# Kernel tuning notes

Measured on AMD Instinct MI355X. Metric: run time of the kernel, lower is better.

Reference implementation:

```python
import jax, jax.numpy as jnp
import numpy as np

B, D, H = 1024, 128, 512


def _made_masks(D, H):
    # Canonical MADE degrees with natural ordering.
    m_in = np.arange(1, D + 1)                       # input degrees 1..D
    m_hid = (np.arange(H) % (D - 1)) + 1             # hidden degrees in [1, D-1]
    m_out = np.concatenate([np.arange(1, D + 1)] * 2)  # output degrees, repeated for (sigma, mu)
    M1 = (m_hid[:, None] >= m_in[None, :]).astype(np.float32)   # [H, D]
    M2 = (m_out[:, None] > m_hid[None, :]).astype(np.float32)   # [2D, H]
    return jnp.asarray(M1), jnp.asarray(M2)


def setup_inputs() -> dict:
    key = jax.random.key(0)
    k1, k2, k3 = jax.random.split(key, 3)
    x = jax.random.normal(k1, (B, D), dtype=jnp.float32)
    # small init so exp(sigma) stays numerically tame
    W1 = jax.random.normal(k2, (H, D), dtype=jnp.float32) * 0.05
    b1 = jnp.zeros((H,), dtype=jnp.float32)
    W2 = jax.random.normal(k3, (2 * D, H), dtype=jnp.float32) * 0.05
    b2 = jnp.zeros((2 * D,), dtype=jnp.float32)
    return {"x": x, "W1": W1, "b1": b1, "W2": W2, "b2": b2}


def reference(x, W1, b1, W2, b2):
    Din = x.shape[1]
    Hid = W1.shape[0]
    M1, M2 = _made_masks(Din, Hid)

    def made(z):
        h = jax.nn.relu(z @ (W1 * M1).T + b1)   # [B, H]
        return h @ (W2 * M2).T + b2              # [B, 2D]

    # backward_flow: sequential inversion, one dim per step (kl_forward=True)
    def step(carry, d):
        z, log_det = carry
        res = made(z)
        sigma = res[:, :Din]
        mu = res[:, Din:]
        s_d = jnp.take(sigma, d, axis=1)
        m_d = jnp.take(mu, d, axis=1)
        x_d = jnp.take(x, d, axis=1)
        z = z.at[:, d].set((x_d - m_d) * jnp.exp(-s_d))
        return (z, log_det - s_d), None

    init = (jnp.zeros_like(x), jnp.zeros((x.shape[0],), dtype=x.dtype))
    (z, log_det), _ = jax.lax.scan(step, init, jnp.arange(Din))
    return z, log_det
```

## Files before the change

kernel.cpp:

```cpp
#include <hip/hip_runtime.h>


#define Bz  1024
#define Dd  128
#define Hh  512
#define HPL 8

typedef float v4f __attribute__((ext_vector_type(4)));

template<int CTRL, int RMASK>
__device__ __forceinline__ float dpp_add(float v) {
    int t = __builtin_amdgcn_update_dpp(0, __float_as_int(v), CTRL, RMASK, 0xf, true);
    return v + __int_as_float(t);
}
__device__ __forceinline__ float wave_sum_bcast(float v) {
    v = dpp_add<0x111, 0xf>(v);
    v = dpp_add<0x112, 0xf>(v);
    v = dpp_add<0x114, 0xf>(v);
    v = dpp_add<0x118, 0xf>(v);
    v = dpp_add<0x142, 0xa>(v);
    v = dpp_add<0x143, 0xc>(v);
    return __int_as_float(__builtin_amdgcn_readlane(__float_as_int(v), 63));
}
__device__ __forceinline__ float bcast_lane(float v, int l) {
    return __int_as_float(__builtin_amdgcn_readlane(__float_as_int(v), l));
}

__global__ void pack_kernel(const float* __restrict__ W1,
                            const float* __restrict__ W2,
                            float* __restrict__ Wp) {
    int idx = blockIdx.x * blockDim.x + threadIdx.x;
    if (idx >= Dd * Hh) return;
    int d = idx >> 9, h = idx & 511;
    int mh = (h % 127) + 1;
    float dot_on = (mh <= d) ? 1.f : 0.f;
    float upd_on = (mh >  d) ? 1.f : 0.f;
    float* bp = Wp + d * 1536;
    bp[h]        = W2[d * Hh + h] * dot_on;
    bp[512 + h]  = W2[(Dd + d) * Hh + h] * dot_on;
    bp[1024 + h] = W1[h * Dd + d] * upd_on;
}

struct WBuf { v4f s0, s1, m0, m1, w0, w1; };

__device__ __forceinline__ void loadbuf(WBuf &b, const float* p) {
    b.s0 = *(const v4f*)(p);
    b.s1 = *(const v4f*)(p + 4);
    b.m0 = *(const v4f*)(p + 512);
    b.m1 = *(const v4f*)(p + 516);
    b.w0 = *(const v4f*)(p + 1024);
    b.w1 = *(const v4f*)(p + 1028);
    __builtin_amdgcn_sched_barrier(0);
}

__device__ __forceinline__ void stepD(int d, int lane,
    float (&a)[HPL], const WBuf &w,
    float xa, float xb, float b2a, float b2b, float b2c, float b2d_,
    float &za, float &zb, float &ld)
{
    float ps0 = 0.f, ps1 = 0.f, pm0 = 0.f, pm1 = 0.f;
#pragma unroll
    for (int k = 0; k < 4; ++k) {
        float h = fmaxf(a[k], 0.f);
        ps0 = fmaf(h, w.s0[k], ps0);
        pm0 = fmaf(h, w.m0[k], pm0);
    }
#pragma unroll
    for (int k = 0; k < 4; ++k) {
        float h = fmaxf(a[4 + k], 0.f);
        ps1 = fmaf(h, w.s1[k], ps1);
        pm1 = fmaf(h, w.m1[k], pm1);
    }
    float ps = wave_sum_bcast(ps0 + ps1);
    float pm = wave_sum_bcast(pm0 + pm1);

    int dl = d & 63;
    float sd = ps + bcast_lane(d < 64 ? b2a : b2b, dl);
    float md = pm + bcast_lane(d < 64 ? b2c : b2d_, dl);
    float xv =      bcast_lane(d < 64 ? xa  : xb,  dl);
    float zd = (xv - md) * __expf(-sd);
    ld -= sd;
    if (dl == lane) { if (d < 64) za = zd; else zb = zd; }

#pragma unroll
    for (int k = 0; k < 4; ++k) a[k]     = fmaf(zd, w.w0[k], a[k]);
#pragma unroll
    for (int k = 0; k < 4; ++k) a[4 + k] = fmaf(zd, w.w1[k], a[4 + k]);
}

__global__ __launch_bounds__(64, 1) void iaf4_kernel(
    const float* __restrict__ x,
    const float* __restrict__ b1,
    const float* __restrict__ b2,
    const float* __restrict__ Wp,
    float* __restrict__ out)
{
    const int lane = (int)threadIdx.x;
    const int row  = (int)blockIdx.x;
    const int h0   = lane * HPL;

    float a[HPL];
    {
        float4 t0 = *(const float4*)(b1 + h0);
        float4 t1 = *(const float4*)(b1 + h0 + 4);
        a[0]=t0.x; a[1]=t0.y; a[2]=t0.z; a[3]=t0.w;
        a[4]=t1.x; a[5]=t1.y; a[6]=t1.z; a[7]=t1.w;
    }
    float xa  = x[row * Dd + lane];
    float xb  = x[row * Dd + 64 + lane];
    float b2a = b2[lane],       b2b = b2[64 + lane];
    float b2c = b2[128 + lane], b2d_ = b2[192 + lane];

    float za = 0.f, zb = 0.f, ld = 0.f;

    const float* base = Wp + h0;
    WBuf A, B, C, D;
    loadbuf(A, base + 0 * 1536);
    loadbuf(B, base + 1 * 1536);
    loadbuf(C, base + 2 * 1536);
    loadbuf(D, base + 3 * 1536);

#pragma unroll 1
    for (int t = 0; t < Dd; t += 4) {
        stepD(t + 0, lane, a, A, xa, xb, b2a, b2b, b2c, b2d_, za, zb, ld);
        loadbuf(A, base + (size_t)((t + 4 < Dd) ? (t + 4) : 0) * 1536);
        stepD(t + 1, lane, a, B, xa, xb, b2a, b2b, b2c, b2d_, za, zb, ld);
        loadbuf(B, base + (size_t)((t + 5 < Dd) ? (t + 5) : 1) * 1536);
        stepD(t + 2, lane, a, C, xa, xb, b2a, b2b, b2c, b2d_, za, zb, ld);
        loadbuf(C, base + (size_t)((t + 6 < Dd) ? (t + 6) : 2) * 1536);
        stepD(t + 3, lane, a, D, xa, xb, b2a, b2b, b2c, b2d_, za, zb, ld);
        loadbuf(D, base + (size_t)((t + 7 < Dd) ? (t + 7) : 3) * 1536);
    }

    out[row * Dd + lane]      = za;
    out[row * Dd + 64 + lane] = zb;
    if (lane == 0) out[Bz * Dd + row] = ld;
}

__global__ __launch_bounds__(64, 1) void iaf_fb_kernel(
    const float* __restrict__ x,  const float* __restrict__ W1,
    const float* __restrict__ b1, const float* __restrict__ W2,
    const float* __restrict__ b2, float* __restrict__ out)
{
    const int lane = (int)threadIdx.x;
    const int row  = (int)blockIdx.x;
    const int h0   = lane * HPL;
    float a[HPL]; int mh[HPL];
#pragma unroll
    for (int k = 0; k < HPL; ++k) { a[k] = b1[h0 + k]; mh[k] = ((h0 + k) % 127) + 1; }
    float xa  = x[row * Dd + lane], xb = x[row * Dd + 64 + lane];
    float b2a = b2[lane], b2b = b2[64 + lane], b2c = b2[128 + lane], b2d_ = b2[192 + lane];
    float za = 0.f, zb = 0.f, ld = 0.f;
    for (int d = 0; d < Dd; ++d) {
        float ps = 0.f, pm = 0.f;
#pragma unroll
        for (int k = 0; k < HPL; ++k) {
            float h = fmaxf(a[k], 0.f);
            h = (mh[k] <= d) ? h : 0.f;
            ps = fmaf(h, W2[d * Hh + h0 + k], ps);
            pm = fmaf(h, W2[(Dd + d) * Hh + h0 + k], pm);
        }
        ps = wave_sum_bcast(ps);
        pm = wave_sum_bcast(pm);
        int dl = d & 63;
        float sd = ps + bcast_lane(d < 64 ? b2a : b2b, dl);
        float md = pm + bcast_lane(d < 64 ? b2c : b2d_, dl);
        float xv =      bcast_lane(d < 64 ? xa  : xb,  dl);
        float zd = (xv - md) * __expf(-sd);
        ld -= sd;
        if (dl == lane) { if (d < 64) za = zd; else zb = zd; }
#pragma unroll
        for (int k = 0; k < HPL; ++k)
            if (d < mh[k]) a[k] = fmaf(zd, W1[(h0 + k) * Dd + d], a[k]);
    }
    out[row * Dd + lane]      = za;
    out[row * Dd + 64 + lane] = zb;
    if (lane == 0) out[Bz * Dd + row] = ld;
}

extern "C" void kernel_launch(void* const* d_in, const int* in_sizes, int n_in,
                              void* d_out, int out_size, void* d_ws, size_t ws_size,
                              hipStream_t stream) {
    const float* x  = (const float*)d_in[0];
    const float* W1 = (const float*)d_in[1];
    const float* b1 = (const float*)d_in[2];
    const float* W2 = (const float*)d_in[3];
    const float* b2 = (const float*)d_in[4];
    float* out = (float*)d_out;
    float* Wp  = (float*)d_ws;

    const size_t need = (size_t)Dd * 1536 * sizeof(float);
    if (ws_size >= need) {
        pack_kernel<<<(Dd * Hh + 255) / 256, 256, 0, stream>>>(W1, W2, Wp);
        iaf4_kernel<<<Bz, 64, 0, stream>>>(x, b1, b2, Wp, out);
    } else {
        iaf_fb_kernel<<<Bz, 64, 0, stream>>>(x, W1, b1, W2, b2, out);
    }
}
```

Measured before the change: 38.72 us.

## Process two batch rows per wave and fold log2 scaling into packed weights

Each 64-lane block now handles two batch rows, so every packed weight load is reused for two independent sequential chains. The two chains interleave their reductions and FMAs, which should hide the latency of the DPP reductions. The sigma weights and biases are pre-scaled by -1/ln2 so the exponential becomes a raw exp2 and the sign flip disappears; log_det is rescaled by ln2 at the end. The cost is half as many blocks (512 on a large GPU, lowering parallelism), more registers per lane, and the prefetch depth drops from four steps to two.

```diff
diff --git a/kernel.cpp b/kernel.cpp
--- a/kernel.cpp
+++ b/kernel.cpp
@@ -5,6 +5,8 @@
 #define Dd  128
 #define Hh  512
 #define HPL 8
+#define LN2 0.6931471805599453f
+#define NEG_RCP_LN2 -1.4426950408889634f
 
 typedef float v4f __attribute__((ext_vector_type(4)));
 
@@ -36,7 +38,7 @@
     float dot_on = (mh <= d) ? 1.f : 0.f;
     float upd_on = (mh >  d) ? 1.f : 0.f;
     float* bp = Wp + d * 1536;
-    bp[h]        = W2[d * Hh + h] * dot_on;
+    bp[h]        = W2[d * Hh + h] * dot_on * NEG_RCP_LN2;
     bp[512 + h]  = W2[(Dd + d) * Hh + h] * dot_on;
     bp[1024 + h] = W1[h * Dd + d] * upd_on;
 }
@@ -53,42 +55,65 @@
     __builtin_amdgcn_sched_barrier(0);
 }
 
-__device__ __forceinline__ void stepD(int d, int lane,
-    float (&a)[HPL], const WBuf &w,
-    float xa, float xb, float b2a, float b2b, float b2c, float b2d_,
-    float &za, float &zb, float &ld)
+__device__ __forceinline__ void stepR2(int d, int lane,
+    float (&a0)[HPL], float (&a1)[HPL], const WBuf &w,
+    float xa0, float xb0, float xa1, float xb1,
+    float b2a, float b2b, float b2c, float b2d_,
+    float &za0, float &zb0, float &za1, float &zb1,
+    float &ld0, float &ld1)
 {
-    float ps0 = 0.f, ps1 = 0.f, pm0 = 0.f, pm1 = 0.f;
-#pragma unroll
-    for (int k = 0; k < 4; ++k) {
-        float h = fmaxf(a[k], 0.f);
-        ps0 = fmaf(h, w.s0[k], ps0);
-        pm0 = fmaf(h, w.m0[k], pm0);
-    }
-#pragma unroll
-    for (int k = 0; k < 4; ++k) {
-        float h = fmaxf(a[4 + k], 0.f);
-        ps1 = fmaf(h, w.s1[k], ps1);
-        pm1 = fmaf(h, w.m1[k], pm1);
-    }
-    float ps = wave_sum_bcast(ps0 + ps1);
-    float pm = wave_sum_bcast(pm0 + pm1);
+    float p00 = 0.f, p01 = 0.f, q00 = 0.f, q01 = 0.f;
+    float p10 = 0.f, p11 = 0.f, q10 = 0.f, q11 = 0.f;
+#pragma unroll
+    for (int k = 0; k < 4; ++k) {
+        float h0 = fmaxf(a0[k], 0.f);
+        float h1 = fmaxf(a1[k], 0.f);
+        p00 = fmaf(h0, w.s0[k], p00);  q00 = fmaf(h0, w.m0[k], q00);
+        p10 = fmaf(h1, w.s0[k], p10);  q10 = fmaf(h1, w.m0[k], q10);
+    }
+#pragma unroll
+    for (int k = 0; k < 4; ++k) {
+        float h0 = fmaxf(a0[4 + k], 0.f);
+        float h1 = fmaxf(a1[4 + k], 0.f);
+        p01 = fmaf(h0, w.s1[k], p01);  q01 = fmaf(h0, w.m1[k], q01);
+        p11 = fmaf(h1, w.s1[k], p11);  q11 = fmaf(h1, w.m1[k], q11);
+    }
+    float sp0 = wave_sum_bcast(p00 + p01);
+    float sm0 = wave_sum_bcast(q00 + q01);
+    float sp1 = wave_sum_bcast(p10 + p11);
+    float sm1 = wave_sum_bcast(q10 + q11);
 
     int dl = d & 63;
-    float sd = ps + bcast_lane(d < 64 ? b2a : b2b, dl);
-    float md = pm + bcast_lane(d < 64 ? b2c : b2d_, dl);
-    float xv =      bcast_lane(d < 64 ? xa  : xb,  dl);
-    float zd = (xv - md) * __expf(-sd);
-    ld -= sd;
-    if (dl == lane) { if (d < 64) za = zd; else zb = zd; }
-
-#pragma unroll
-    for (int k = 0; k < 4; ++k) a[k]     = fmaf(zd, w.w0[k], a[k]);
-#pragma unroll
-    for (int k = 0; k < 4; ++k) a[4 + k] = fmaf(zd, w.w1[k], a[4 + k]);
-}
-
-__global__ __launch_bounds__(64, 1) void iaf4_kernel(
+    float bs  = bcast_lane(d < 64 ? b2a : b2b, dl);
+    float bm  = bcast_lane(d < 64 ? b2c : b2d_, dl);
+    float xv0 = bcast_lane(d < 64 ? xa0 : xb0, dl);
+    float xv1 = bcast_lane(d < 64 ? xa1 : xb1, dl);
+
+    float s0 = sp0 + bs, s1 = sp1 + bs;
+    float m0 = sm0 + bm, m1 = sm1 + bm;
+    float e0 = __builtin_amdgcn_exp2f(s0);
+    float e1 = __builtin_amdgcn_exp2f(s1);
+    float zd0 = (xv0 - m0) * e0;
+    float zd1 = (xv1 - m1) * e1;
+    ld0 += s0;
+    ld1 += s1;
+    if (dl == lane) {
+        if (d < 64) { za0 = zd0; za1 = zd1; }
+        else        { zb0 = zd0; zb1 = zd1; }
+    }
+#pragma unroll
+    for (int k = 0; k < 4; ++k) {
+        a0[k] = fmaf(zd0, w.w0[k], a0[k]);
+        a1[k] = fmaf(zd1, w.w0[k], a1[k]);
+    }
+#pragma unroll
+    for (int k = 0; k < 4; ++k) {
+        a0[4 + k] = fmaf(zd0, w.w1[k], a0[4 + k]);
+        a1[4 + k] = fmaf(zd1, w.w1[k], a1[4 + k]);
+    }
+}
+
+__global__ __launch_bounds__(64, 1) void iaf5_kernel(
     const float* __restrict__ x,
     const float* __restrict__ b1,
     const float* __restrict__ b2,
@@ -96,45 +121,51 @@
     float* __restrict__ out)
 {
     const int lane = (int)threadIdx.x;
-    const int row  = (int)blockIdx.x;
+    const int r0   = (int)blockIdx.x * 2;
+    const int r1   = r0 + 1;
     const int h0   = lane * HPL;
 
-    float a[HPL];
+    float a0[HPL], a1[HPL];
     {
         float4 t0 = *(const float4*)(b1 + h0);
         float4 t1 = *(const float4*)(b1 + h0 + 4);
-        a[0]=t0.x; a[1]=t0.y; a[2]=t0.z; a[3]=t0.w;
-        a[4]=t1.x; a[5]=t1.y; a[6]=t1.z; a[7]=t1.w;
-    }
-    float xa  = x[row * Dd + lane];
-    float xb  = x[row * Dd + 64 + lane];
-    float b2a = b2[lane],       b2b = b2[64 + lane];
-    float b2c = b2[128 + lane], b2d_ = b2[192 + lane];
-
-    float za = 0.f, zb = 0.f, ld = 0.f;
+        a0[0]=t0.x; a0[1]=t0.y; a0[2]=t0.z; a0[3]=t0.w;
+        a0[4]=t1.x; a0[5]=t1.y; a0[6]=t1.z; a0[7]=t1.w;
+#pragma unroll
+        for (int k = 0; k < HPL; ++k) a1[k] = a0[k];
+    }
+    float xa0 = x[r0 * Dd + lane],      xb0 = x[r0 * Dd + 64 + lane];
+    float xa1 = x[r1 * Dd + lane],      xb1 = x[r1 * Dd + 64 + lane];
+    float b2a = b2[lane] * NEG_RCP_LN2;
+    float b2b = b2[64 + lane] * NEG_RCP_LN2;
+    float b2c = b2[128 + lane],         b2d_ = b2[192 + lane];
+
+    float za0 = 0.f, zb0 = 0.f, za1 = 0.f, zb1 = 0.f;
+    float ld0 = 0.f, ld1 = 0.f;
 
     const float* base = Wp + h0;
-    WBuf A, B, C, D;
-    loadbuf(A, base + 0 * 1536);
-    loadbuf(B, base + 1 * 1536);
-    loadbuf(C, base + 2 * 1536);
-    loadbuf(D, base + 3 * 1536);
+    WBuf A, B;
+    loadbuf(A, base);
+    loadbuf(B, base + 1536);
 
 #pragma unroll 1
-    for (int t = 0; t < Dd; t += 4) {
-        stepD(t + 0, lane, a, A, xa, xb, b2a, b2b, b2c, b2d_, za, zb, ld);
-        loadbuf(A, base + (size_t)((t + 4 < Dd) ? (t + 4) : 0) * 1536);
-        stepD(t + 1, lane, a, B, xa, xb, b2a, b2b, b2c, b2d_, za, zb, ld);
-        loadbuf(B, base + (size_t)((t + 5 < Dd) ? (t + 5) : 1) * 1536);
-        stepD(t + 2, lane, a, C, xa, xb, b2a, b2b, b2c, b2d_, za, zb, ld);
-        loadbuf(C, base + (size_t)((t + 6 < Dd) ? (t + 6) : 2) * 1536);
-        stepD(t + 3, lane, a, D, xa, xb, b2a, b2b, b2c, b2d_, za, zb, ld);
-        loadbuf(D, base + (size_t)((t + 7 < Dd) ? (t + 7) : 3) * 1536);
-    }
-
-    out[row * Dd + lane]      = za;
-    out[row * Dd + 64 + lane] = zb;
-    if (lane == 0) out[Bz * Dd + row] = ld;
+    for (int t = 0; t < Dd; t += 2) {
+        stepR2(t, lane, a0, a1, A, xa0, xb0, xa1, xb1,
+               b2a, b2b, b2c, b2d_, za0, zb0, za1, zb1, ld0, ld1);
+        loadbuf(A, base + (size_t)((t + 2 < Dd) ? (t + 2) : 0) * 1536);
+        stepR2(t + 1, lane, a0, a1, B, xa0, xb0, xa1, xb1,
+               b2a, b2b, b2c, b2d_, za0, zb0, za1, zb1, ld0, ld1);
+        loadbuf(B, base + (size_t)((t + 3 < Dd) ? (t + 3) : 1) * 1536);
+    }
+
+    out[r0 * Dd + lane]      = za0;
+    out[r0 * Dd + 64 + lane] = zb0;
+    out[r1 * Dd + lane]      = za1;
+    out[r1 * Dd + 64 + lane] = zb1;
+    if (lane == 0) {
+        out[Bz * Dd + r0] = LN2 * ld0;
+        out[Bz * Dd + r1] = LN2 * ld1;
+    }
 }
 
 __global__ __launch_bounds__(64, 1) void iaf_fb_kernel(
@@ -192,7 +223,7 @@
     const size_t need = (size_t)Dd * 1536 * sizeof(float);
     if (ws_size >= need) {
         pack_kernel<<<(Dd * Hh + 255) / 256, 256, 0, stream>>>(W1, W2, Wp);
-        iaf4_kernel<<<Bz, 64, 0, stream>>>(x, b1, b2, Wp, out);
+        iaf5_kernel<<<Bz / 2, 64, 0, stream>>>(x, b1, b2, Wp, out);
     } else {
         iaf_fb_kernel<<<Bz, 64, 0, stream>>>(x, W1, b1, W2, b2, out);
     }
```

Result: slower. 60.43 us (+56.1%).

## Stream packed weights through LDS via async global_load_lds with swizzled layout

Applied to the files above, without the earlier changes.

Replaces the register-buffered weight prefetch with a 4-deep LDS ring filled by direct global-to-LDS loads, waiting on vmcnt each step. The pack kernel now emits a swizzled layout so LDS reads avoid bank conflicts, and folds -log2(e) into the sigma weights and biases so exp becomes a native exp2 with the log-det rescaled once at the end. The aim is to free VGPRs and hide global-load latency in the serial 128-step loop. In exchange it depends on a hand-tuned waitcnt count and uses 24KB of LDS per block.

```diff
diff --git a/kernel.cpp b/kernel.cpp
--- a/kernel.cpp
+++ b/kernel.cpp
@@ -1,12 +1,16 @@
 #include <hip/hip_runtime.h>
+#include <stdint.h>
 
 
 #define Bz  1024
 #define Dd  128
 #define Hh  512
-#define HPL 8
+#define LN2 0.6931471805599453f
+#define NRL -1.4426950408889634f
 
 typedef float v4f __attribute__((ext_vector_type(4)));
+typedef const __attribute__((address_space(1))) uint32_t* gas_t;
+typedef __attribute__((address_space(3))) uint32_t* las_t;
 
 template<int CTRL, int RMASK>
 __device__ __forceinline__ float dpp_add(float v) {
@@ -30,76 +34,32 @@
                             const float* __restrict__ W2,
                             float* __restrict__ Wp) {
     int idx = blockIdx.x * blockDim.x + threadIdx.x;
-    if (idx >= Dd * Hh) return;
-    int d = idx >> 9, h = idx & 511;
+    if (idx >= Dd * 1536) return;
+    int d = idx / 1536, f = idx % 1536;
+    int seg = f >> 9, h = f & 511;
     int mh = (h % 127) + 1;
-    float dot_on = (mh <= d) ? 1.f : 0.f;
-    float upd_on = (mh >  d) ? 1.f : 0.f;
-    float* bp = Wp + d * 1536;
-    bp[h]        = W2[d * Hh + h] * dot_on;
-    bp[512 + h]  = W2[(Dd + d) * Hh + h] * dot_on;
-    bp[1024 + h] = W1[h * Dd + d] * upd_on;
-}
-
-struct WBuf { v4f s0, s1, m0, m1, w0, w1; };
-
-__device__ __forceinline__ void loadbuf(WBuf &b, const float* p) {
-    b.s0 = *(const v4f*)(p);
-    b.s1 = *(const v4f*)(p + 4);
-    b.m0 = *(const v4f*)(p + 512);
-    b.m1 = *(const v4f*)(p + 516);
-    b.w0 = *(const v4f*)(p + 1024);
-    b.w1 = *(const v4f*)(p + 1028);
-    __builtin_amdgcn_sched_barrier(0);
-}
-
-__device__ __forceinline__ void stepD(int d, int lane,
-    float (&a)[HPL], const WBuf &w,
-    float xa, float xb, float b2a, float b2b, float b2c, float b2d_,
-    float &za, float &zb, float &ld)
-{
-    float ps0 = 0.f, ps1 = 0.f, pm0 = 0.f, pm1 = 0.f;
-#pragma unroll
-    for (int k = 0; k < 4; ++k) {
-        float h = fmaxf(a[k], 0.f);
-        ps0 = fmaf(h, w.s0[k], ps0);
-        pm0 = fmaf(h, w.m0[k], pm0);
-    }
-#pragma unroll
-    for (int k = 0; k < 4; ++k) {
-        float h = fmaxf(a[4 + k], 0.f);
-        ps1 = fmaf(h, w.s1[k], ps1);
-        pm1 = fmaf(h, w.m1[k], pm1);
-    }
-    float ps = wave_sum_bcast(ps0 + ps1);
-    float pm = wave_sum_bcast(pm0 + pm1);
-
-    int dl = d & 63;
-    float sd = ps + bcast_lane(d < 64 ? b2a : b2b, dl);
-    float md = pm + bcast_lane(d < 64 ? b2c : b2d_, dl);
-    float xv =      bcast_lane(d < 64 ? xa  : xb,  dl);
-    float zd = (xv - md) * __expf(-sd);
-    ld -= sd;
-    if (dl == lane) { if (d < 64) za = zd; else zb = zd; }
-
-#pragma unroll
-    for (int k = 0; k < 4; ++k) a[k]     = fmaf(zd, w.w0[k], a[k]);
-#pragma unroll
-    for (int k = 0; k < 4; ++k) a[4 + k] = fmaf(zd, w.w1[k], a[4 + k]);
-}
-
-__global__ __launch_bounds__(64, 1) void iaf4_kernel(
+    float v;
+    if (seg == 0)      v = W2[d * Hh + h]        * ((mh <= d) ? NRL : 0.f);
+    else if (seg == 1) v = W2[(Dd + d) * Hh + h] * ((mh <= d) ? 1.f : 0.f);
+    else               v = W1[h * Dd + d]        * ((mh >  d) ? 1.f : 0.f);
+    int c = (f >> 2) & 127, e = f & 3;
+    int pos = (seg << 7) + (c & ~1) + ((c & 1) ^ ((c >> 3) & 1));
+    Wp[d * 1536 + pos * 4 + e] = v;
+}
+
+__global__ __launch_bounds__(64, 1) void iaf6_kernel(
     const float* __restrict__ x,
     const float* __restrict__ b1,
     const float* __restrict__ b2,
     const float* __restrict__ Wp,
     float* __restrict__ out)
 {
+    __shared__ float lds[4 * 1536];
     const int lane = (int)threadIdx.x;
     const int row  = (int)blockIdx.x;
-    const int h0   = lane * HPL;
-
-    float a[HPL];
+    const int h0   = lane * 8;
+
+    float a[8];
     {
         float4 t0 = *(const float4*)(b1 + h0);
         float4 t1 = *(const float4*)(b1 + h0 + 4);
@@ -108,33 +68,77 @@
     }
     float xa  = x[row * Dd + lane];
     float xb  = x[row * Dd + 64 + lane];
-    float b2a = b2[lane],       b2b = b2[64 + lane];
-    float b2c = b2[128 + lane], b2d_ = b2[192 + lane];
-
-    float za = 0.f, zb = 0.f, ld = 0.f;
-
-    const float* base = Wp + h0;
-    WBuf A, B, C, D;
-    loadbuf(A, base + 0 * 1536);
-    loadbuf(B, base + 1 * 1536);
-    loadbuf(C, base + 2 * 1536);
-    loadbuf(D, base + 3 * 1536);
+    float b2a = b2[lane] * NRL,        b2b = b2[64 + lane] * NRL;
+    float b2c = b2[128 + lane],        b2d_ = b2[192 + lane];
+    asm volatile("" : "+v"(xa), "+v"(xb), "+v"(b2a), "+v"(b2b), "+v"(b2c),
+                      "+v"(b2d_), "+v"(a[0]), "+v"(a[1]), "+v"(a[2]),
+                      "+v"(a[3]), "+v"(a[4]), "+v"(a[5]), "+v"(a[6]), "+v"(a[7]));
+
+    auto stage = [&](int t) {
+        const float* g = Wp + (size_t)t * 1536 + lane * 4;
+        float* lb = lds + (t & 3) * 1536;
+#pragma unroll
+        for (int i = 0; i < 6; ++i)
+            __builtin_amdgcn_global_load_lds((gas_t)(g + i * 256),
+                                             (las_t)(lb + i * 256), 16, 0, 0);
+    };
+
+    stage(0); stage(1); stage(2); stage(3);
+
+    float za = 0.f, zb = 0.f, ldet = 0.f;
+    const int bit = (lane >> 2) & 1;
+    const int p0  = 2 * lane + bit;
+    const int p1  = 2 * lane + 1 - bit;
 
 #pragma unroll 1
-    for (int t = 0; t < Dd; t += 4) {
-        stepD(t + 0, lane, a, A, xa, xb, b2a, b2b, b2c, b2d_, za, zb, ld);
-        loadbuf(A, base + (size_t)((t + 4 < Dd) ? (t + 4) : 0) * 1536);
-        stepD(t + 1, lane, a, B, xa, xb, b2a, b2b, b2c, b2d_, za, zb, ld);
-        loadbuf(B, base + (size_t)((t + 5 < Dd) ? (t + 5) : 1) * 1536);
-        stepD(t + 2, lane, a, C, xa, xb, b2a, b2b, b2c, b2d_, za, zb, ld);
-        loadbuf(C, base + (size_t)((t + 6 < Dd) ? (t + 6) : 2) * 1536);
-        stepD(t + 3, lane, a, D, xa, xb, b2a, b2b, b2c, b2d_, za, zb, ld);
-        loadbuf(D, base + (size_t)((t + 7 < Dd) ? (t + 7) : 3) * 1536);
+    for (int t = 0; t < Dd; ++t) {
+        asm volatile("s_waitcnt vmcnt(18)" ::: "memory");
+        __builtin_amdgcn_sched_barrier(0);
+
+        const v4f* lp = (const v4f*)(lds + (t & 3) * 1536);
+        v4f s0 = lp[p0],       s1 = lp[p1];
+        v4f m0 = lp[128 + p0], m1 = lp[128 + p1];
+        v4f w0 = lp[256 + p0], w1 = lp[256 + p1];
+
+        float ps0 = 0.f, ps1 = 0.f, pm0 = 0.f, pm1 = 0.f;
+#pragma unroll
+        for (int k = 0; k < 4; ++k) {
+            float hv = fmaxf(a[k], 0.f);
+            ps0 = fmaf(hv, s0[k], ps0);
+            pm0 = fmaf(hv, m0[k], pm0);
+        }
+#pragma unroll
+        for (int k = 0; k < 4; ++k) {
+            float hv = fmaxf(a[4 + k], 0.f);
+            ps1 = fmaf(hv, s1[k], ps1);
+            pm1 = fmaf(hv, m1[k], pm1);
+        }
+        float sp = wave_sum_bcast(ps0 + ps1);
+        float sm = wave_sum_bcast(pm0 + pm1);
+
+        int dl = t & 63;
+        float bs = bcast_lane(t < 64 ? b2a : b2b, dl);
+        float bm = bcast_lane(t < 64 ? b2c : b2d_, dl);
+        float xv = bcast_lane(t < 64 ? xa  : xb,  dl);
+
+        float sd = sp + bs;
+        float zd = (xv - (sm + bm)) * __builtin_amdgcn_exp2f(sd);
+        ldet += sd;
+        if (dl == lane) { if (t < 64) za = zd; else zb = zd; }
+
+#pragma unroll
+        for (int k = 0; k < 4; ++k) a[k]     = fmaf(zd, w0[k], a[k]);
+#pragma unroll
+        for (int k = 0; k < 4; ++k) a[4 + k] = fmaf(zd, w1[k], a[4 + k]);
+
+        __builtin_amdgcn_sched_barrier(0);
+        asm volatile("s_waitcnt lgkmcnt(0)" ::: "memory");
+        if (t < Dd - 4) stage(t + 4);
     }
 
     out[row * Dd + lane]      = za;
     out[row * Dd + 64 + lane] = zb;
-    if (lane == 0) out[Bz * Dd + row] = ld;
+    if (lane == 0) out[Bz * Dd + row] = LN2 * ldet;
 }
 
 __global__ __launch_bounds__(64, 1) void iaf_fb_kernel(
@@ -144,17 +148,17 @@
 {
     const int lane = (int)threadIdx.x;
     const int row  = (int)blockIdx.x;
-    const int h0   = lane * HPL;
-    float a[HPL]; int mh[HPL];
-#pragma unroll
-    for (int k = 0; k < HPL; ++k) { a[k] = b1[h0 + k]; mh[k] = ((h0 + k) % 127) + 1; }
+    const int h0   = lane * 8;
+    float a[8]; int mh[8];
+#pragma unroll
+    for (int k = 0; k < 8; ++k) { a[k] = b1[h0 + k]; mh[k] = ((h0 + k) % 127) + 1; }
     float xa  = x[row * Dd + lane], xb = x[row * Dd + 64 + lane];
     float b2a = b2[lane], b2b = b2[64 + lane], b2c = b2[128 + lane], b2d_ = b2[192 + lane];
     float za = 0.f, zb = 0.f, ld = 0.f;
     for (int d = 0; d < Dd; ++d) {
         float ps = 0.f, pm = 0.f;
 #pragma unroll
-        for (int k = 0; k < HPL; ++k) {
+        for (int k = 0; k < 8; ++k) {
             float h = fmaxf(a[k], 0.f);
             h = (mh[k] <= d) ? h : 0.f;
             ps = fmaf(h, W2[d * Hh + h0 + k], ps);
@@ -170,7 +174,7 @@
         ld -= sd;
         if (dl == lane) { if (d < 64) za = zd; else zb = zd; }
 #pragma unroll
-        for (int k = 0; k < HPL; ++k)
+        for (int k = 0; k < 8; ++k)
             if (d < mh[k]) a[k] = fmaf(zd, W1[(h0 + k) * Dd + d], a[k]);
     }
     out[row * Dd + lane]      = za;
@@ -191,8 +195,8 @@
 
     const size_t need = (size_t)Dd * 1536 * sizeof(float);
     if (ws_size >= need) {
-        pack_kernel<<<(Dd * Hh + 255) / 256, 256, 0, stream>>>(W1, W2, Wp);
-        iaf4_kernel<<<Bz, 64, 0, stream>>>(x, b1, b2, Wp, out);
+        pack_kernel<<<(Dd * 1536 + 255) / 256, 256, 0, stream>>>(W1, W2, Wp);
+        iaf6_kernel<<<Bz, 64, 0, stream>>>(x, b1, b2, Wp, out);
     } else {
         iaf_fb_kernel<<<Bz, 64, 0, stream>>>(x, W1, b1, W2, b2, out);
     }
```

Result: slower. 53.15 us (+37.3%).

## Fold biases and exp scaling into packed weights and use packed FMAs

Applied to the files above, without the earlier changes.

The pack kernel now pre-scales the sigma weights by -log2(e) and the W1 update weights by exp(-b2[d]). This lets the serial loop work in the base-2 domain with no per-step bias broadcasts, and the per-dim exp(-b2) factor and the log-det bias sum are applied once at the end. The inner dot and update loops are also rewritten with 2-wide vector FMAs so the compiler can emit packed fp32 instructions. Together these shorten the latency-bound serial chain per dimension, at the cost of slightly different floating-point rounding.

```diff
diff --git a/kernel.cpp b/kernel.cpp
--- a/kernel.cpp
+++ b/kernel.cpp
@@ -1,12 +1,18 @@
 #include <hip/hip_runtime.h>
+#include <stdint.h>
 
 
 #define Bz  1024
 #define Dd  128
 #define Hh  512
-#define HPL 8
+#define LN2 0.6931471805599453f
+#define NRL -1.4426950408889634f
 
 typedef float v4f __attribute__((ext_vector_type(4)));
+typedef float v2f __attribute__((ext_vector_type(2)));
+
+#define LOQ(q) __builtin_shufflevector(q, q, 0, 1)
+#define HIQ(q) __builtin_shufflevector(q, q, 2, 3)
 
 template<int CTRL, int RMASK>
 __device__ __forceinline__ float dpp_add(float v) {
@@ -28,17 +34,16 @@
 
 __global__ void pack_kernel(const float* __restrict__ W1,
                             const float* __restrict__ W2,
+                            const float* __restrict__ b2,
                             float* __restrict__ Wp) {
     int idx = blockIdx.x * blockDim.x + threadIdx.x;
     if (idx >= Dd * Hh) return;
     int d = idx >> 9, h = idx & 511;
     int mh = (h % 127) + 1;
-    float dot_on = (mh <= d) ? 1.f : 0.f;
-    float upd_on = (mh >  d) ? 1.f : 0.f;
     float* bp = Wp + d * 1536;
-    bp[h]        = W2[d * Hh + h] * dot_on;
-    bp[512 + h]  = W2[(Dd + d) * Hh + h] * dot_on;
-    bp[1024 + h] = W1[h * Dd + d] * upd_on;
+    bp[h]        = W2[d * Hh + h] * ((mh <= d) ? NRL : 0.f);
+    bp[512 + h]  = W2[(Dd + d) * Hh + h] * ((mh <= d) ? 1.f : 0.f);
+    bp[1024 + h] = W1[h * Dd + d] * ((mh > d) ? __expf(-b2[d]) : 0.f);
 }
 
 struct WBuf { v4f s0, s1, m0, m1, w0, w1; };
@@ -53,42 +58,45 @@
     __builtin_amdgcn_sched_barrier(0);
 }
 
-__device__ __forceinline__ void stepD(int d, int lane,
-    float (&a)[HPL], const WBuf &w,
-    float xa, float xb, float b2a, float b2b, float b2c, float b2d_,
-    float &za, float &zb, float &ld)
+__device__ __forceinline__ void stepD(int u, int lane,
+    v2f (&a2)[4], const WBuf &w, float xa, float xb,
+    float &za, float &zb, float &ldet)
 {
-    float ps0 = 0.f, ps1 = 0.f, pm0 = 0.f, pm1 = 0.f;
-#pragma unroll
-    for (int k = 0; k < 4; ++k) {
-        float h = fmaxf(a[k], 0.f);
-        ps0 = fmaf(h, w.s0[k], ps0);
-        pm0 = fmaf(h, w.m0[k], pm0);
-    }
-#pragma unroll
-    for (int k = 0; k < 4; ++k) {
-        float h = fmaxf(a[4 + k], 0.f);
-        ps1 = fmaf(h, w.s1[k], ps1);
-        pm1 = fmaf(h, w.m1[k], pm1);
-    }
-    float ps = wave_sum_bcast(ps0 + ps1);
-    float pm = wave_sum_bcast(pm0 + pm1);
-
-    int dl = d & 63;
-    float sd = ps + bcast_lane(d < 64 ? b2a : b2b, dl);
-    float md = pm + bcast_lane(d < 64 ? b2c : b2d_, dl);
-    float xv =      bcast_lane(d < 64 ? xa  : xb,  dl);
-    float zd = (xv - md) * __expf(-sd);
-    ld -= sd;
-    if (dl == lane) { if (d < 64) za = zd; else zb = zd; }
-
-#pragma unroll
-    for (int k = 0; k < 4; ++k) a[k]     = fmaf(zd, w.w0[k], a[k]);
-#pragma unroll
-    for (int k = 0; k < 4; ++k) a[4 + k] = fmaf(zd, w.w1[k], a[4 + k]);
-}
-
-__global__ __launch_bounds__(64, 1) void iaf4_kernel(
+    const v2f zz = {0.f, 0.f};
+    v2f h0 = __builtin_elementwise_max(a2[0], zz);
+    v2f h1 = __builtin_elementwise_max(a2[1], zz);
+    v2f h2 = __builtin_elementwise_max(a2[2], zz);
+    v2f h3 = __builtin_elementwise_max(a2[3], zz);
+
+    v2f psA = zz, psB = zz, pmA = zz, pmB = zz;
+    psA = __builtin_elementwise_fma(h0, (v2f)LOQ(w.s0), psA);
+    pmA = __builtin_elementwise_fma(h0, (v2f)LOQ(w.m0), pmA);
+    psB = __builtin_elementwise_fma(h1, (v2f)HIQ(w.s0), psB);
+    pmB = __builtin_elementwise_fma(h1, (v2f)HIQ(w.m0), pmB);
+    psA = __builtin_elementwise_fma(h2, (v2f)LOQ(w.s1), psA);
+    pmA = __builtin_elementwise_fma(h2, (v2f)LOQ(w.m1), pmA);
+    psB = __builtin_elementwise_fma(h3, (v2f)HIQ(w.s1), psB);
+    pmB = __builtin_elementwise_fma(h3, (v2f)HIQ(w.m1), pmB);
+    v2f psp = psA + psB;
+    v2f pmp = pmA + pmB;
+
+    float sp = wave_sum_bcast(psp.x + psp.y);
+    float sm = wave_sum_bcast(pmp.x + pmp.y);
+
+    int dl = u & 63;
+    float xv = bcast_lane(u < 64 ? xa : xb, dl);
+    float zd = (xv - sm) * __builtin_amdgcn_exp2f(sp);
+    ldet += sp;
+    if (dl == lane) { if (u < 64) za = zd; else zb = zd; }
+
+    v2f zd2 = {zd, zd};
+    a2[0] = __builtin_elementwise_fma(zd2, (v2f)LOQ(w.w0), a2[0]);
+    a2[1] = __builtin_elementwise_fma(zd2, (v2f)HIQ(w.w0), a2[1]);
+    a2[2] = __builtin_elementwise_fma(zd2, (v2f)LOQ(w.w1), a2[2]);
+    a2[3] = __builtin_elementwise_fma(zd2, (v2f)HIQ(w.w1), a2[3]);
+}
+
+__global__ __launch_bounds__(64, 1) void iaf12_kernel(
     const float* __restrict__ x,
     const float* __restrict__ b1,
     const float* __restrict__ b2,
@@ -97,21 +105,24 @@
 {
     const int lane = (int)threadIdx.x;
     const int row  = (int)blockIdx.x;
-    const int h0   = lane * HPL;
-
-    float a[HPL];
+    const int h0   = lane * 8;
+
+    v2f a2[4];
     {
-        float4 t0 = *(const float4*)(b1 + h0);
-        float4 t1 = *(const float4*)(b1 + h0 + 4);
-        a[0]=t0.x; a[1]=t0.y; a[2]=t0.z; a[3]=t0.w;
-        a[4]=t1.x; a[5]=t1.y; a[6]=t1.z; a[7]=t1.w;
-    }
-    float xa  = x[row * Dd + lane];
-    float xb  = x[row * Dd + 64 + lane];
-    float b2a = b2[lane],       b2b = b2[64 + lane];
-    float b2c = b2[128 + lane], b2d_ = b2[192 + lane];
-
-    float za = 0.f, zb = 0.f, ld = 0.f;
+        v4f t0v = *(const v4f*)(b1 + h0);
+        v4f t1v = *(const v4f*)(b1 + h0 + 4);
+        a2[0] = LOQ(t0v); a2[1] = HIQ(t0v);
+        a2[2] = LOQ(t1v); a2[3] = HIQ(t1v);
+    }
+    float bsa = b2[lane],       bsb = b2[64 + lane];
+    float bma = b2[128 + lane], bmb = b2[192 + lane];
+    float xa  = x[row * Dd + lane]      - bma;
+    float xb  = x[row * Dd + 64 + lane] - bmb;
+    float Ea  = __builtin_amdgcn_exp2f(bsa * NRL);
+    float Eb  = __builtin_amdgcn_exp2f(bsb * NRL);
+    float Csum = NRL * wave_sum_bcast(bsa + bsb);
+
+    float za = 0.f, zb = 0.f, ldet = 0.f;
 
     const float* base = Wp + h0;
     WBuf A, B, C, D;
@@ -122,19 +133,19 @@
 
 #pragma unroll 1
     for (int t = 0; t < Dd; t += 4) {
-        stepD(t + 0, lane, a, A, xa, xb, b2a, b2b, b2c, b2d_, za, zb, ld);
+        stepD(t + 0, lane, a2, A, xa, xb, za, zb, ldet);
         loadbuf(A, base + (size_t)((t + 4 < Dd) ? (t + 4) : 0) * 1536);
-        stepD(t + 1, lane, a, B, xa, xb, b2a, b2b, b2c, b2d_, za, zb, ld);
+        stepD(t + 1, lane, a2, B, xa, xb, za, zb, ldet);
         loadbuf(B, base + (size_t)((t + 5 < Dd) ? (t + 5) : 1) * 1536);
-        stepD(t + 2, lane, a, C, xa, xb, b2a, b2b, b2c, b2d_, za, zb, ld);
+        stepD(t + 2, lane, a2, C, xa, xb, za, zb, ldet);
         loadbuf(C, base + (size_t)((t + 6 < Dd) ? (t + 6) : 2) * 1536);
-        stepD(t + 3, lane, a, D, xa, xb, b2a, b2b, b2c, b2d_, za, zb, ld);
+        stepD(t + 3, lane, a2, D, xa, xb, za, zb, ldet);
         loadbuf(D, base + (size_t)((t + 7 < Dd) ? (t + 7) : 3) * 1536);
     }
 
-    out[row * Dd + lane]      = za;
-    out[row * Dd + 64 + lane] = zb;
-    if (lane == 0) out[Bz * Dd + row] = ld;
+    out[row * Dd + lane]      = za * Ea;
+    out[row * Dd + 64 + lane] = zb * Eb;
+    if (lane == 0) out[Bz * Dd + row] = LN2 * (ldet + Csum);
 }
 
 __global__ __launch_bounds__(64, 1) void iaf_fb_kernel(
@@ -144,17 +155,17 @@
 {
     const int lane = (int)threadIdx.x;
     const int row  = (int)blockIdx.x;
-    const int h0   = lane * HPL;
-    float a[HPL]; int mh[HPL];
+    const int h0   = lane * 8;
+    float a[8]; int mh[8];
 #pragma unroll
-    for (int k = 0; k < HPL; ++k) { a[k] = b1[h0 + k]; mh[k] = ((h0 + k) % 127) + 1; }
+    for (int k = 0; k < 8; ++k) { a[k] = b1[h0 + k]; mh[k] = ((h0 + k) % 127) + 1; }
     float xa  = x[row * Dd + lane], xb = x[row * Dd + 64 + lane];
     float b2a = b2[lane], b2b = b2[64 + lane], b2c = b2[128 + lane], b2d_ = b2[192 + lane];
     float za = 0.f, zb = 0.f, ld = 0.f;
     for (int d = 0; d < Dd; ++d) {
         float ps = 0.f, pm = 0.f;
 #pragma unroll
-        for (int k = 0; k < HPL; ++k) {
+        for (int k = 0; k < 8; ++k) {
             float h = fmaxf(a[k], 0.f);
             h = (mh[k] <= d) ? h : 0.f;
             ps = fmaf(h, W2[d * Hh + h0 + k], ps);
@@ -170,7 +181,7 @@
         ld -= sd;
         if (dl == lane) { if (d < 64) za = zd; else zb = zd; }
 #pragma unroll
-        for (int k = 0; k < HPL; ++k)
+        for (int k = 0; k < 8; ++k)
             if (d < mh[k]) a[k] = fmaf(zd, W1[(h0 + k) * Dd + d], a[k]);
     }
     out[row * Dd + lane]      = za;
@@ -191,8 +202,8 @@
 
     const size_t need = (size_t)Dd * 1536 * sizeof(float);
     if (ws_size >= need) {
-        pack_kernel<<<(Dd * Hh + 255) / 256, 256, 0, stream>>>(W1, W2, Wp);
-        iaf4_kernel<<<Bz, 64, 0, stream>>>(x, b1, b2, Wp, out);
+        pack_kernel<<<(Dd * Hh + 255) / 256, 256, 0, stream>>>(W1, W2, b2, Wp);
+        iaf12_kernel<<<Bz, 64, 0, stream>>>(x, b1, b2, Wp, out);
     } else {
         iaf_fb_kernel<<<Bz, 64, 0, stream>>>(x, W1, b1, W2, b2, out);
     }
```

Result: faster. 33.12 us (-14.5%).
